# Kernel tuning notes

Measured on AMD Instinct MI355X. Metric: run time of the kernel, lower is better.

The kernel has to match this reference:

```python
import jax, jax.numpy as jnp
import numpy as np

B, S, E = 2, 2048, 1024
H = 16
D = E // H  # head_dim = 64


def setup_inputs() -> dict:
    key = jax.random.key(0)
    ks = jax.random.split(key, 11)
    s = 1.0 / np.sqrt(E)
    return {
        "x": jax.random.normal(ks[0], (B, S, E), dtype=jnp.float32),
        "Wq": jax.random.uniform(ks[1], (E, E), jnp.float32, -s, s),
        "bq": jnp.zeros((E,), jnp.float32),
        "Wk": jax.random.uniform(ks[2], (E, E), jnp.float32, -s, s),
        "bk": jnp.zeros((E,), jnp.float32),
        "Wv": jax.random.uniform(ks[3], (E, E), jnp.float32, -s, s),
        "bv": jnp.zeros((E,), jnp.float32),
        "Wo": jax.random.uniform(ks[4], (E, E), jnp.float32, -s, s),
        "bo": jnp.zeros((E,), jnp.float32),
        "J_attn": jax.random.normal(ks[5], (H, D, D), jnp.float32) * 0.02,
        "lambda_attn": jnp.float32(0.5),
    }


def reference(x, Wq, bq, Wk, bk, Wv, bv, Wo, bo, J_attn, lambda_attn):
    b, s, _ = x.shape
    scale = jnp.sqrt(jnp.float32(D))

    def split_heads(y):  # [b,s,E] -> [b,H,s,D]
        return y.reshape(b, s, H, D).transpose(0, 2, 1, 3)

    Q = split_heads(x @ Wq.T + bq)
    K = split_heads(x @ Wk.T + bk)
    V = split_heads(x @ Wv.T + bv)

    attn_scores = jnp.einsum('bhid,bhjd->bhij', Q, K) / scale

    Qn = jnp.tanh(Q)
    Kn = jnp.tanh(K)
    # fold J into Qn first (small [H,D,D] contraction), then one big matmul
    QJ = jnp.einsum('bhid,hde->bhie', Qn, J_attn)
    delta = jnp.einsum('bhie,bhje->bhij', QJ, Kn)

    attn_scores = attn_scores + lambda_attn * delta
    attn_probs = jax.nn.softmax(attn_scores, axis=-1)

    out = jnp.einsum('bhij,bhjd->bhid', attn_probs, V)
    out = out.transpose(0, 2, 1, 3).reshape(b, s, E)
    return out @ Wo.T + bo
```

## Files before the change

### kernel.cpp

```cpp
#include <hip/hip_runtime.h>
#include <math.h>

#define NH 16

typedef __bf16 bf16x8 __attribute__((ext_vector_type(8)));
typedef float f32x4 __attribute__((ext_vector_type(4)));

__device__ __forceinline__ unsigned short f2bf(float f) {
  unsigned u = __float_as_uint(f);
  u += 0x7fffu + ((u >> 16) & 1u);
  return (unsigned short)(u >> 16);
}
__device__ __forceinline__ float bf2f(unsigned short h) {
  return __uint_as_float(((unsigned)h) << 16);
}
__device__ __forceinline__ float fexp2(float x) {
  return __builtin_amdgcn_exp2f(x);
}
__device__ __forceinline__ float fast_tanh16(float x) {
  return 1.f - 2.f * __builtin_amdgcn_rcpf(fexp2(16.f * x) + 1.f);
}
__device__ __forceinline__ void gl_lds16(const void* g, void* l) {
  __builtin_amdgcn_global_load_lds((const __attribute__((address_space(1))) void*)g,
                                   (__attribute__((address_space(3))) void*)l, 16, 0, 0);
}
union Frag8 { bf16x8 v; unsigned short u[8]; };
union FragU { bf16x8 v; unsigned u[4]; };
union FragQ { bf16x8 v; unsigned long long q[2]; };

__global__ __launch_bounds__(256) void prep_all(const float* __restrict__ x,
                                                const float* __restrict__ Wq,
                                                const float* __restrict__ Wk,
                                                const float* __restrict__ Wv,
                                                const float* __restrict__ Wo,
                                                unsigned short* __restrict__ xh,
                                                unsigned short* __restrict__ wcat3,
                                                unsigned short* __restrict__ wocat)
{
  const int bid = blockIdx.x, tid = threadIdx.x;
  if (bid < 4096) {
    int i = bid * 256 + tid;
    float4 v = *(const float4*)&x[(size_t)i*4];
    ushort4 o;
    o.x = f2bf(v.x); o.y = f2bf(v.y); o.z = f2bf(v.z); o.w = f2bf(v.w);
    *(ushort4*)&xh[(size_t)i*4] = o;
  } else if (bid < 7168) {
    int i = (bid - 4096) * 256 + tid;
    int sel = i >> 18, loc = i & 262143;
    const float* src = (sel == 0) ? Wq : (sel == 1) ? Wk : Wv;
    float4 v = *(const float4*)&src[(size_t)loc*4];
    ushort4 o;
    o.x = f2bf(v.x); o.y = f2bf(v.y); o.z = f2bf(v.z); o.w = f2bf(v.w);
    *(ushort4*)&wcat3[(size_t)i*4] = o;
  } else {
    int i = (bid - 7168) * 256 + tid;
    int r = i >> 8, c = i & 255;
    float4 v = *(const float4*)&Wo[(size_t)r*1024 + c*4];
    ushort4 hi, lo;
    hi.x = f2bf(v.x); lo.x = f2bf(v.x - bf2f(hi.x));
    hi.y = f2bf(v.y); lo.y = f2bf(v.y - bf2f(hi.y));
    hi.z = f2bf(v.z); lo.z = f2bf(v.z - bf2f(hi.z));
    hi.w = f2bf(v.w); lo.w = f2bf(v.w - bf2f(hi.w));
    *(ushort4*)&wocat[(size_t)r*2048 + c*4]        = hi;
    *(ushort4*)&wocat[(size_t)r*2048 + 1024 + c*4] = lo;
  }
}

__global__ __launch_bounds__(256) void prep_jt(const float* __restrict__ J,
                                               const float* __restrict__ lam_p,
                                               unsigned short* __restrict__ Jt)
{
  __shared__ float T[64][65];
  const int h = blockIdx.x, tid = threadIdx.x;
  const float lam = lam_p[0] * 1.44269504f;
#pragma unroll
  for (int c = 0; c < 4; ++c) {
    int i = tid + c*256;
    int d = i >> 4, e4 = i & 15;
    float4 v = *(const float4*)&J[(size_t)h*4096 + d*64 + e4*4];
    T[d][e4*4+0] = v.x; T[d][e4*4+1] = v.y; T[d][e4*4+2] = v.z; T[d][e4*4+3] = v.w;
  }
  __syncthreads();
  const int e = tid >> 2, d0 = (tid & 3) * 16;
#pragma unroll
  for (int j4 = 0; j4 < 4; ++j4) {
    ushort4 o;
    o.x = f2bf(lam * T[d0+j4*4+0][e]);
    o.y = f2bf(lam * T[d0+j4*4+1][e]);
    o.z = f2bf(lam * T[d0+j4*4+2][e]);
    o.w = f2bf(lam * T[d0+j4*4+3][e]);
    *(ushort4*)&Jt[((size_t)h*64 + e)*64 + d0 + j4*4] = o;
  }
}

__global__ __launch_bounds__(256) void gemm_qkv(const unsigned short* __restrict__ A,
                                                const unsigned short* __restrict__ W,
                                                const float* __restrict__ bq,
                                                const float* __restrict__ bk,
                                                const float* __restrict__ bv,
                                                unsigned short* __restrict__ Qcat,
                                                unsigned short* __restrict__ Kcat,
                                                unsigned short* __restrict__ Vt)
{
  __shared__ unsigned short S[16384];
  const int tid = threadIdx.x, lane = tid & 63, wq = tid >> 6;
  const int l15 = lane & 15, lq = lane >> 4;
  const int n0 = blockIdx.x * 128, m0 = blockIdx.y * 128;
  const int wr = (wq & 1) * 64, wc = (wq >> 1) * 64;
  const int mode = n0 >> 10;

  f32x4 acc[4][4];
#pragma unroll
  for (int mb = 0; mb < 4; ++mb)
#pragma unroll
    for (int nb = 0; nb < 4; ++nb) { f32x4 z = {0.f,0.f,0.f,0.f}; acc[mb][nb] = z; }

  const unsigned short* mat = (wq < 2) ? A : W;
  const int rbase = (wq < 2) ? m0 : n0;
  unsigned short* lbase = S + (wq >> 1) * 8192;
  const int srow = lane >> 3, sslot = lane & 7;

  for (int k0 = 0; k0 < 1024; k0 += 64) {
    __syncthreads();
#pragma unroll
    for (int t = 0; t < 8; ++t) {
      int row = (wq & 1) * 64 + t*8 + srow;
      int chunk = sslot ^ (row & 7);
      gl_lds16(mat + (size_t)(rbase + row)*1024 + k0 + chunk*8,
               lbase + ((wq & 1) * 64 + t*8) * 64);
    }
    __syncthreads();
#pragma unroll
    for (int kk = 0; kk < 2; ++kk) {
      int c = kk*4 + lq;
      bf16x8 af[4], bf_[4];
#pragma unroll
      for (int mb = 0; mb < 4; ++mb) {
        int m = wr + mb*16 + l15;
        af[mb] = *(const bf16x8*)&S[m*64 + (c ^ (m & 7))*8];
      }
#pragma unroll
      for (int nb = 0; nb < 4; ++nb) {
        int n = wc + nb*16 + l15;
        bf_[nb] = *(const bf16x8*)&S[8192 + n*64 + (c ^ (n & 7))*8];
      }
#pragma unroll
      for (int mb = 0; mb < 4; ++mb)
#pragma unroll
        for (int nb = 0; nb < 4; ++nb)
          acc[mb][nb] = __builtin_amdgcn_mfma_f32_16x16x32_bf16(af[mb], bf_[nb], acc[mb][nb], 0,0,0);
    }
  }

  const float* bias = (mode == 0) ? bq : (mode == 1) ? bk : bv;
  float bvv[4];
#pragma unroll
  for (int nb = 0; nb < 4; ++nb) bvv[nb] = bias[((n0 & 1023) + wc + nb*16 + l15)];

  if (mode == 2) {
#pragma unroll
    for (int mb = 0; mb < 4; ++mb) {
      int mrow = m0 + wr + mb*16 + lq*4;
      int b = mrow >> 11, s0 = mrow & 2047;
#pragma unroll
      for (int nb = 0; nb < 4; ++nb) {
        int n = (n0 & 1023) + wc + nb*16 + l15;
        int h = n >> 6, d = n & 63;
        ushort4 o;
        o.x = f2bf(acc[mb][nb][0] + bvv[nb]);
        o.y = f2bf(acc[mb][nb][1] + bvv[nb]);
        o.z = f2bf(acc[mb][nb][2] + bvv[nb]);
        o.w = f2bf(acc[mb][nb][3] + bvv[nb]);
        *(ushort4*)&Vt[((size_t)(b*NH + h)*64 + d)*2048 + s0] = o;
      }
    }
    return;
  }

#pragma unroll
  for (int mb = 0; mb < 4; ++mb) {
#pragma unroll
    for (int r = 0; r < 4; ++r) {
      int m = m0 + wr + mb*16 + lq*4 + r;
      int b = m >> 11, s = m & 2047;
#pragma unroll
      for (int nb = 0; nb < 4; ++nb) {
        float v = acc[mb][nb][r] + bvv[nb];
        int n = (n0 & 1023) + wc + nb*16 + l15;
        int h = n >> 6, d = n & 63;
        size_t row = ((size_t)(b*NH + h)*2048 + s)*128;
        if (mode == 0) {
          Qcat[row + d] = f2bf(v * 0.18033688f);
        } else {
          Kcat[row + d]      = f2bf(v);
          Kcat[row + 64 + d] = f2bf(1.f - 2.f * __builtin_amdgcn_rcpf(__expf(2.f*v) + 1.f));
        }
      }
    }
  }
}

__global__ __launch_bounds__(256) void build_qj2(unsigned short* __restrict__ Qcat,
                                                 const unsigned short* __restrict__ Jt)
{
  const int tid = threadIdx.x, lane = tid & 63, wq = tid >> 6;
  const int l15 = lane & 15, lq = lane >> 4;
  const int bh = blockIdx.y, row0 = blockIdx.x * 128;
  const int h = bh & (NH-1);

  bf16x8 jf[4][2];
#pragma unroll
  for (int nb = 0; nb < 4; ++nb)
#pragma unroll
    for (int kst = 0; kst < 2; ++kst)
      jf[nb][kst] = *(const bf16x8*)&Jt[((size_t)h*64 + nb*16 + l15)*64 + kst*32 + lq*8];

  Frag8 af[2][2];
#pragma unroll
  for (int mb = 0; mb < 2; ++mb) {
    const unsigned short* qp = Qcat + ((size_t)(bh*2048 + row0 + wq*32 + mb*16 + l15))*128 + lq*8;
#pragma unroll
    for (int kst = 0; kst < 2; ++kst) {
      Frag8 raw;
      raw.v = *(const bf16x8*)(qp + kst*32);
#pragma unroll
      for (int j = 0; j < 8; ++j) {
        float t = fast_tanh16(bf2f(raw.u[j]));
        af[mb][kst].u[j] = (unsigned short)(__float_as_uint(t) >> 16);
      }
    }
  }

  f32x4 acc[2][4];
#pragma unroll
  for (int mb = 0; mb < 2; ++mb)
#pragma unroll
    for (int nb = 0; nb < 4; ++nb) { f32x4 z = {0.f,0.f,0.f,0.f}; acc[mb][nb] = z; }
#pragma unroll
  for (int kst = 0; kst < 2; ++kst)
#pragma unroll
    for (int mb = 0; mb < 2; ++mb)
#pragma unroll
      for (int nb = 0; nb < 4; ++nb)
        acc[mb][nb] = __builtin_amdgcn_mfma_f32_16x16x32_bf16(af[mb][kst].v, jf[nb][kst], acc[mb][nb], 0,0,0);

#pragma unroll
  for (int mb = 0; mb < 2; ++mb)
#pragma unroll
    for (int r = 0; r < 4; ++r) {
      size_t rowb = ((size_t)(bh*2048 + row0 + wq*32 + mb*16 + lq*4 + r))*128 + 64;
#pragma unroll
      for (int nb = 0; nb < 4; ++nb)
        Qcat[rowb + nb*16 + l15] = f2bf(acc[mb][nb][r]);
    }
}

__global__ __launch_bounds__(256, 4) void flash7(
    const unsigned short* __restrict__ Qcat, const unsigned short* __restrict__ Kcat,
    const unsigned short* __restrict__ Vt, float* __restrict__ OP0,
    float* __restrict__ OP1, float* __restrict__ OP2, float* __restrict__ lpart)
{
  __shared__ unsigned short Ks[64*128];
  __shared__ unsigned short Vs[64*64];
  const int tid = threadIdx.x, lane = tid & 63, wq = tid >> 6;
  const int l15 = lane & 15, lq = lane >> 4;
  const int bid = blockIdx.x;
  const int bh = (((bid >> 3) & 3) << 3) | (bid & 7);
  const int inner = bid >> 5;
  const int row0 = (inner & 15) * 128;
  const int ks = inner >> 4;
  const int jt0 = ks * 11;
  const int jtN = jt0 + ((ks < 2) ? 11 : 10);

  Frag8 qf[2][4];
#pragma unroll
  for (int nb = 0; nb < 2; ++nb) {
    const unsigned short* qp = Qcat + ((size_t)(bh*2048 + row0 + wq*32 + nb*16 + l15))*128 + lq*8;
#pragma unroll
    for (int kst = 0; kst < 4; ++kst)
      qf[nb][kst].v = *(const bf16x8*)(qp + kst*32);
  }

  FragU ones;
  ones.u[0] = 0x3F803F80u; ones.u[1] = 0x3F803F80u;
  ones.u[2] = 0x3F803F80u; ones.u[3] = 0x3F803F80u;

  f32x4 o[4][2];
  f32x4 lacc[2];
  { f32x4 z = {0.f,0.f,0.f,0.f}; lacc[0] = z; lacc[1] = z; }
#pragma unroll
  for (int db = 0; db < 4; ++db)
#pragma unroll
    for (int nb = 0; nb < 2; ++nb) { f32x4 z = {0.f,0.f,0.f,0.f}; o[db][nb] = z; }

  const unsigned short* kgb = Kcat + ((size_t)bh*2048)*128;
  const unsigned short* vg  = Vt + (size_t)bh*64*2048;

  for (int jt = jt0; jt < jtN; ++jt) {
    __syncthreads();
#pragma unroll
    for (int t = 0; t < 4; ++t) {
      int g = (wq*4 + t)*4 + (lane >> 4);
      int slot = lane & 15;
      int chunk = (slot & 8) | ((slot ^ g) & 7);
      gl_lds16(kgb + (size_t)(jt*64 + g)*128 + chunk*8, Ks + (wq*4 + t)*512);
    }
#pragma unroll
    for (int t = 0; t < 2; ++t) {
      int rv = (wq*2 + t)*8 + (lane >> 3);
      int chunk = (lane & 7) ^ (rv & 7);
      gl_lds16(vg + (size_t)rv*2048 + jt*64 + chunk*8, Vs + (wq*2 + t)*512);
    }
    __syncthreads();

#pragma unroll
    for (int t = 0; t < 2; ++t) {
      unsigned P2[2][2][2];
#pragma unroll
      for (int kk = 0; kk < 2; ++kk) {
        const int kb = 2*t + kk;
        bf16x8 af[4];
#pragma unroll
        for (int kst = 0; kst < 4; ++kst) {
          int key = kb*16 + l15;
          int c = kst*4 + lq;
          int slot = (c & 8) | ((c ^ key) & 7);
          af[kst] = *(const bf16x8*)&Ks[key*128 + slot*8];
        }
        f32x4 s[2];
        { f32x4 z = {0.f,0.f,0.f,0.f}; s[0] = z; s[1] = z; }
#pragma unroll
        for (int kst = 0; kst < 4; ++kst) {
          s[0] = __builtin_amdgcn_mfma_f32_16x16x32_bf16(af[kst], qf[0][kst].v, s[0], 0,0,0);
          s[1] = __builtin_amdgcn_mfma_f32_16x16x32_bf16(af[kst], qf[1][kst].v, s[1], 0,0,0);
        }
#pragma unroll
        for (int nb = 0; nb < 2; ++nb) {
          float e0 = fexp2(s[nb][0]), e1 = fexp2(s[nb][1]);
          float e2 = fexp2(s[nb][2]), e3 = fexp2(s[nb][3]);
          P2[nb][kk][0] = __builtin_amdgcn_perm(__float_as_uint(e1), __float_as_uint(e0), 0x07060302u);
          P2[nb][kk][1] = __builtin_amdgcn_perm(__float_as_uint(e3), __float_as_uint(e2), 0x07060302u);
        }
      }

      FragU bfr[2];
#pragma unroll
      for (int nb = 0; nb < 2; ++nb) {
        bfr[nb].u[0] = P2[nb][0][0];
        bfr[nb].u[1] = P2[nb][0][1];
        bfr[nb].u[2] = P2[nb][1][0];
        bfr[nb].u[3] = P2[nb][1][1];
      }
      lacc[0] = __builtin_amdgcn_mfma_f32_16x16x32_bf16(ones.v, bfr[0].v, lacc[0], 0,0,0);
      lacc[1] = __builtin_amdgcn_mfma_f32_16x16x32_bf16(ones.v, bfr[1].v, lacc[1], 0,0,0);

      const int c0 = 4*t + (lq >> 1);
      const int woff = 4*(lq & 1);
#pragma unroll
      for (int db = 0; db < 4; ++db) {
        int d = db*16 + l15;
        FragQ va;
        va.q[0] = *(const unsigned long long*)&Vs[d*64 + ((c0     ^ (d & 7))*8) + woff];
        va.q[1] = *(const unsigned long long*)&Vs[d*64 + (((c0+2) ^ (d & 7))*8) + woff];
        o[db][0] = __builtin_amdgcn_mfma_f32_16x16x32_bf16(va.v, bfr[0].v, o[db][0], 0,0,0);
        o[db][1] = __builtin_amdgcn_mfma_f32_16x16x32_bf16(va.v, bfr[1].v, o[db][1], 0,0,0);
      }
    }
  }

  float* OP = (ks == 0) ? OP0 : (ks == 1) ? OP1 : OP2;
#pragma unroll
  for (int nb = 0; nb < 2; ++nb) {
    int qrow = row0 + wq*32 + nb*16 + l15;
    if (lq == 0) lpart[(size_t)ks*65536 + bh*2048 + qrow] = lacc[nb][0];
#pragma unroll
    for (int db = 0; db < 4; ++db)
#pragma unroll
      for (int r = 0; r < 4; ++r) {
        int d = db*16 + lq*4 + r;
        OP[(size_t)(bh*64 + d)*2048 + qrow] = o[db][nb][r];
      }
  }
}

__global__ __launch_bounds__(256) void combine3(const float* __restrict__ OP0,
                                                const float* __restrict__ OP1,
                                                const float* __restrict__ OP2,
                                                const float* __restrict__ lpart,
                                                unsigned short* __restrict__ attcat)
{
  __shared__ float Ts[64*68];
  __shared__ float Ls[64];
  const int tid = threadIdx.x;
  const int bh = blockIdx.y, s0 = blockIdx.x * 64;
  const int b = bh >> 4, h = bh & (NH-1);
#pragma unroll
  for (int c = 0; c < 4; ++c) {
    int fid = tid + c*256;
    int d = fid >> 4, s4 = fid & 15;
    size_t gi = ((size_t)(bh*64 + d))*2048 + s0 + s4*4;
    float4 a = *(const float4*)&OP0[gi];
    float4 bb = *(const float4*)&OP1[gi];
    float4 cc = *(const float4*)&OP2[gi];
    Ts[(s4*4+0)*68 + d] = a.x + bb.x + cc.x;
    Ts[(s4*4+1)*68 + d] = a.y + bb.y + cc.y;
    Ts[(s4*4+2)*68 + d] = a.z + bb.z + cc.z;
    Ts[(s4*4+3)*68 + d] = a.w + bb.w + cc.w;
  }
  if (tid < 64) {
    size_t li = (size_t)bh*2048 + s0 + tid;
    Ls[tid] = lpart[li] + lpart[65536 + li] + lpart[131072 + li];
  }
  __syncthreads();
  const int sl = tid >> 2, d0 = (tid & 3) * 16;
  const float inv = 1.f / Ls[sl];
  const size_t rb = ((size_t)(b*2048 + s0 + sl))*2048 + h*64;
#pragma unroll
  for (int j4 = 0; j4 < 4; ++j4) {
    float4 t = *(const float4*)&Ts[sl*68 + d0 + j4*4];
    float v0 = t.x*inv, v1 = t.y*inv, v2 = t.z*inv, v3 = t.w*inv;
    ushort4 hi, lo;
    hi.x = f2bf(v0); lo.x = f2bf(v0 - bf2f(hi.x));
    hi.y = f2bf(v1); lo.y = f2bf(v1 - bf2f(hi.y));
    hi.z = f2bf(v2); lo.z = f2bf(v2 - bf2f(hi.z));
    hi.w = f2bf(v3); lo.w = f2bf(v3 - bf2f(hi.w));
    *(ushort4*)&attcat[rb + d0 + j4*4]        = hi;
    *(ushort4*)&attcat[rb + 1024 + d0 + j4*4] = lo;
  }
}

__global__ __launch_bounds__(512) void gemm3b(const unsigned short* __restrict__ A,
                                              const unsigned short* __restrict__ W,
                                              const float* __restrict__ bias,
                                              float* __restrict__ out)
{
  __shared__ unsigned short S[65536];
  const int tid = threadIdx.x, lane = tid & 63, wid = tid >> 6;
  const int l15 = lane & 15, lq = lane >> 4;
  const int n0 = blockIdx.x * 128, m0 = blockIdx.y * 128;
  const int wrow = wid >> 2, wcol = wid & 3;

  f32x4 acc[4][2];
#pragma unroll
  for (int mb = 0; mb < 4; ++mb)
#pragma unroll
    for (int nb = 0; nb < 2; ++nb) { f32x4 z = {0.f,0.f,0.f,0.f}; acc[mb][nb] = z; }

  const int region = wid >> 1;
  const unsigned short* mat = (region < 2) ? A : W;
  const int rbase = (region < 2) ? m0 : n0;
  const int koff  = (region & 1) * 1024;
  const int rhalf = (wid & 1) * 64;
  const int srow = lane >> 3, sslot = lane & 7;

  auto STAGE = [&](int buf, int k0) {
    unsigned short* lb = S + buf*32768 + region*8192 + rhalf*64;
#pragma unroll
    for (int t = 0; t < 8; ++t) {
      int row = rhalf + t*8 + srow;
      int chunk = sslot ^ (row & 7);
      gl_lds16(mat + (size_t)(rbase + row)*2048 + koff + k0 + chunk*8,
               lb + t*512);
    }
  };

  int cur = 0;
  STAGE(0, 0);
  __syncthreads();

  for (int k0 = 0; k0 < 1024; k0 += 64) {
    if (k0 + 64 < 1024) STAGE(cur ^ 1, k0 + 64);
    const unsigned short* Sc = S + cur*32768;
#pragma unroll
    for (int kk = 0; kk < 2; ++kk) {
      int c = kk*4 + lq;
      bf16x8 ah[4], al[4], bh_[2], bl_[2];
#pragma unroll
      for (int mb = 0; mb < 4; ++mb) {
        int m = wrow*64 + mb*16 + l15;
        int so = (c ^ (m & 7))*8;
        ah[mb] = *(const bf16x8*)&Sc[m*64 + so];
        al[mb] = *(const bf16x8*)&Sc[8192 + m*64 + so];
      }
#pragma unroll
      for (int nb = 0; nb < 2; ++nb) {
        int n = wcol*32 + nb*16 + l15;
        int so = (c ^ (n & 7))*8;
        bh_[nb] = *(const bf16x8*)&Sc[16384 + n*64 + so];
        bl_[nb] = *(const bf16x8*)&Sc[24576 + n*64 + so];
      }
#pragma unroll
      for (int mb = 0; mb < 4; ++mb)
#pragma unroll
        for (int nb = 0; nb < 2; ++nb) {
          acc[mb][nb] = __builtin_amdgcn_mfma_f32_16x16x32_bf16(ah[mb], bh_[nb], acc[mb][nb], 0,0,0);
          acc[mb][nb] = __builtin_amdgcn_mfma_f32_16x16x32_bf16(al[mb], bh_[nb], acc[mb][nb], 0,0,0);
          acc[mb][nb] = __builtin_amdgcn_mfma_f32_16x16x32_bf16(ah[mb], bl_[nb], acc[mb][nb], 0,0,0);
        }
    }
    __syncthreads();
    cur ^= 1;
  }

  float bvv[2];
#pragma unroll
  for (int nb = 0; nb < 2; ++nb) bvv[nb] = bias[n0 + wcol*32 + nb*16 + l15];
#pragma unroll
  for (int mb = 0; mb < 4; ++mb)
#pragma unroll
    for (int r = 0; r < 4; ++r) {
      int m = m0 + wrow*64 + mb*16 + lq*4 + r;
#pragma unroll
      for (int nb = 0; nb < 2; ++nb) {
        int n = n0 + wcol*32 + nb*16 + l15;
        out[(size_t)m*1024 + n] = acc[mb][nb][r] + bvv[nb];
      }
    }
}

extern "C" void kernel_launch(void* const* d_in, const int* in_sizes, int n_in,
                              void* d_out, int out_size, void* d_ws, size_t ws_size,
                              hipStream_t stream)
{
  const float* x   = (const float*)d_in[0];
  const float* Wq  = (const float*)d_in[1];
  const float* bq  = (const float*)d_in[2];
  const float* Wk  = (const float*)d_in[3];
  const float* bk  = (const float*)d_in[4];
  const float* Wv  = (const float*)d_in[5];
  const float* bv  = (const float*)d_in[6];
  const float* Wo  = (const float*)d_in[7];
  const float* bo  = (const float*)d_in[8];
  const float* J   = (const float*)d_in[9];
  const float* lam = (const float*)d_in[10];

  char* p = (char*)d_ws;
  char* regionA = p;
  unsigned short* xh     = (unsigned short*)p;  p += (size_t)4096*1024*2;
  unsigned short* wcat3  = (unsigned short*)p;  p += (size_t)3072*1024*2;
  unsigned short* Jt     = (unsigned short*)p;  p += (size_t)16*64*64*2;
  p += (size_t)2*1024*1024;
  unsigned short* Qcat   = (unsigned short*)p;  p += (size_t)65536*128*2;
  unsigned short* Kcat   = (unsigned short*)p;  p += (size_t)65536*128*2;
  unsigned short* Vt     = (unsigned short*)p;  p += (size_t)32*64*2048*2;
  unsigned short* wocat  = (unsigned short*)p;  p += (size_t)1024*2048*2;
  unsigned short* attcat = (unsigned short*)p;  p += (size_t)4096*2048*2;
  float*          OP0    = (float*)p;           p += (size_t)32*64*2048*4;
  float*          OP1    = (float*)p;           p += (size_t)32*64*2048*4;
  float*          lpart  = (float*)p;           p += (size_t)3*65536*4;
  float*          OP2    = (float*)regionA;
  float* out = (float*)d_out;

  dim3 blk(256);

  prep_all<<<dim3(8192), blk, 0, stream>>>(x, Wq, Wk, Wv, Wo, xh, wcat3, wocat);
  prep_jt<<<dim3(16), blk, 0, stream>>>(J, lam, Jt);
  gemm_qkv<<<dim3(24, 32), blk, 0, stream>>>(xh, wcat3, bq, bk, bv, Qcat, Kcat, Vt);
  build_qj2<<<dim3(16, 32), blk, 0, stream>>>(Qcat, Jt);
  flash7<<<dim3(1536), blk, 0, stream>>>(Qcat, Kcat, Vt, OP0, OP1, OP2, lpart);
  combine3<<<dim3(32, 32), blk, 0, stream>>>(OP0, OP1, OP2, lpart, attcat);
  gemm3b<<<dim3(8, 32), dim3(512), 0, stream>>>(attcat, wocat, bo, out);
}
```

Before: 247.3 us.

## Double-buffer QKV GEMM and flash LDS tiles, fold prep_jt into prep_all

Result: faster. 240.3 us (-2.8%).

```diff
diff --git a/kernel.cpp b/kernel.cpp
--- a/kernel.cpp
+++ b/kernel.cpp
@@ -33,11 +33,38 @@
                                                 const float* __restrict__ Wk,
                                                 const float* __restrict__ Wv,
                                                 const float* __restrict__ Wo,
+                                                const float* __restrict__ J,
+                                                const float* __restrict__ lam_p,
                                                 unsigned short* __restrict__ xh,
                                                 unsigned short* __restrict__ wcat3,
-                                                unsigned short* __restrict__ wocat)
-{
+                                                unsigned short* __restrict__ wocat,
+                                                unsigned short* __restrict__ Jt)
+{
+  __shared__ float T[64][65];
   const int bid = blockIdx.x, tid = threadIdx.x;
+  if (bid >= 8192) {
+    const int h = bid - 8192;
+    const float lam = lam_p[0] * 1.44269504f;
+#pragma unroll
+    for (int c = 0; c < 4; ++c) {
+      int i = tid + c*256;
+      int d = i >> 4, e4 = i & 15;
+      float4 v = *(const float4*)&J[(size_t)h*4096 + d*64 + e4*4];
+      T[d][e4*4+0] = v.x; T[d][e4*4+1] = v.y; T[d][e4*4+2] = v.z; T[d][e4*4+3] = v.w;
+    }
+    __syncthreads();
+    const int e = tid >> 2, d0 = (tid & 3) * 16;
+#pragma unroll
+    for (int j4 = 0; j4 < 4; ++j4) {
+      ushort4 o;
+      o.x = f2bf(lam * T[d0+j4*4+0][e]);
+      o.y = f2bf(lam * T[d0+j4*4+1][e]);
+      o.z = f2bf(lam * T[d0+j4*4+2][e]);
+      o.w = f2bf(lam * T[d0+j4*4+3][e]);
+      *(ushort4*)&Jt[((size_t)h*64 + e)*64 + d0 + j4*4] = o;
+    }
+    return;
+  }
   if (bid < 4096) {
     int i = bid * 256 + tid;
     float4 v = *(const float4*)&x[(size_t)i*4];
@@ -66,34 +93,7 @@
   }
 }
 
-__global__ __launch_bounds__(256) void prep_jt(const float* __restrict__ J,
-                                               const float* __restrict__ lam_p,
-                                               unsigned short* __restrict__ Jt)
-{
-  __shared__ float T[64][65];
-  const int h = blockIdx.x, tid = threadIdx.x;
-  const float lam = lam_p[0] * 1.44269504f;
-#pragma unroll
-  for (int c = 0; c < 4; ++c) {
-    int i = tid + c*256;
-    int d = i >> 4, e4 = i & 15;
-    float4 v = *(const float4*)&J[(size_t)h*4096 + d*64 + e4*4];
-    T[d][e4*4+0] = v.x; T[d][e4*4+1] = v.y; T[d][e4*4+2] = v.z; T[d][e4*4+3] = v.w;
-  }
-  __syncthreads();
-  const int e = tid >> 2, d0 = (tid & 3) * 16;
-#pragma unroll
-  for (int j4 = 0; j4 < 4; ++j4) {
-    ushort4 o;
-    o.x = f2bf(lam * T[d0+j4*4+0][e]);
-    o.y = f2bf(lam * T[d0+j4*4+1][e]);
-    o.z = f2bf(lam * T[d0+j4*4+2][e]);
-    o.w = f2bf(lam * T[d0+j4*4+3][e]);
-    *(ushort4*)&Jt[((size_t)h*64 + e)*64 + d0 + j4*4] = o;
-  }
-}
-
-__global__ __launch_bounds__(256) void gemm_qkv(const unsigned short* __restrict__ A,
+__global__ __launch_bounds__(512) void gemm_qkv(const unsigned short* __restrict__ A,
                                                 const unsigned short* __restrict__ W,
                                                 const float* __restrict__ bq,
                                                 const float* __restrict__ bk,
@@ -102,69 +102,78 @@
                                                 unsigned short* __restrict__ Kcat,
                                                 unsigned short* __restrict__ Vt)
 {
-  __shared__ unsigned short S[16384];
-  const int tid = threadIdx.x, lane = tid & 63, wq = tid >> 6;
+  __shared__ unsigned short S[32768];
+  const int tid = threadIdx.x, lane = tid & 63, wid = tid >> 6;
   const int l15 = lane & 15, lq = lane >> 4;
   const int n0 = blockIdx.x * 128, m0 = blockIdx.y * 128;
-  const int wr = (wq & 1) * 64, wc = (wq >> 1) * 64;
+  const int wrow = wid >> 2, wcol = wid & 3;
   const int mode = n0 >> 10;
 
-  f32x4 acc[4][4];
+  f32x4 acc[4][2];
 #pragma unroll
   for (int mb = 0; mb < 4; ++mb)
 #pragma unroll
-    for (int nb = 0; nb < 4; ++nb) { f32x4 z = {0.f,0.f,0.f,0.f}; acc[mb][nb] = z; }
-
-  const unsigned short* mat = (wq < 2) ? A : W;
-  const int rbase = (wq < 2) ? m0 : n0;
-  unsigned short* lbase = S + (wq >> 1) * 8192;
+    for (int nb = 0; nb < 2; ++nb) { f32x4 z = {0.f,0.f,0.f,0.f}; acc[mb][nb] = z; }
+
+  const int region = wid >> 2, quarter = wid & 3;
+  const unsigned short* mat = (region == 0) ? A : W;
+  const int rbase = (region == 0) ? m0 : n0;
   const int srow = lane >> 3, sslot = lane & 7;
 
+  auto STAGE = [&](int buf, int k0) {
+    unsigned short* lb = S + buf*16384 + region*8192 + quarter*2048;
+#pragma unroll
+    for (int t = 0; t < 4; ++t) {
+      int row = quarter*32 + t*8 + srow;
+      int chunk = sslot ^ (row & 7);
+      gl_lds16(mat + (size_t)(rbase + row)*1024 + k0 + chunk*8, lb + t*512);
+    }
+  };
+
+  int cur = 0;
+  STAGE(0, 0);
+  __syncthreads();
+
   for (int k0 = 0; k0 < 1024; k0 += 64) {
-    __syncthreads();
-#pragma unroll
-    for (int t = 0; t < 8; ++t) {
-      int row = (wq & 1) * 64 + t*8 + srow;
-      int chunk = sslot ^ (row & 7);
-      gl_lds16(mat + (size_t)(rbase + row)*1024 + k0 + chunk*8,
-               lbase + ((wq & 1) * 64 + t*8) * 64);
-    }
-    __syncthreads();
+    if (k0 + 64 < 1024) STAGE(cur ^ 1, k0 + 64);
+    const unsigned short* Sc = S + cur*16384;
 #pragma unroll
     for (int kk = 0; kk < 2; ++kk) {
       int c = kk*4 + lq;
-      bf16x8 af[4], bf_[4];
+      bf16x8 af[4], bf_[2];
 #pragma unroll
       for (int mb = 0; mb < 4; ++mb) {
-        int m = wr + mb*16 + l15;
-        af[mb] = *(const bf16x8*)&S[m*64 + (c ^ (m & 7))*8];
-      }
-#pragma unroll
-      for (int nb = 0; nb < 4; ++nb) {
-        int n = wc + nb*16 + l15;
-        bf_[nb] = *(const bf16x8*)&S[8192 + n*64 + (c ^ (n & 7))*8];
+        int m = wrow*64 + mb*16 + l15;
+        af[mb] = *(const bf16x8*)&Sc[m*64 + (c ^ (m & 7))*8];
+      }
+#pragma unroll
+      for (int nb = 0; nb < 2; ++nb) {
+        int n = wcol*32 + nb*16 + l15;
+        bf_[nb] = *(const bf16x8*)&Sc[8192 + n*64 + (c ^ (n & 7))*8];
       }
 #pragma unroll
       for (int mb = 0; mb < 4; ++mb)
 #pragma unroll
-        for (int nb = 0; nb < 4; ++nb)
+        for (int nb = 0; nb < 2; ++nb)
           acc[mb][nb] = __builtin_amdgcn_mfma_f32_16x16x32_bf16(af[mb], bf_[nb], acc[mb][nb], 0,0,0);
     }
+    __syncthreads();
+    cur ^= 1;
   }
 
   const float* bias = (mode == 0) ? bq : (mode == 1) ? bk : bv;
-  float bvv[4];
-#pragma unroll
-  for (int nb = 0; nb < 4; ++nb) bvv[nb] = bias[((n0 & 1023) + wc + nb*16 + l15)];
+  float bvv[2];
+#pragma unroll
+  for (int nb = 0; nb < 2; ++nb) bvv[nb] = bias[((n0 & 1023) + wcol*32 + nb*16 + l15)];
 
   if (mode == 2) {
 #pragma unroll
     for (int mb = 0; mb < 4; ++mb) {
-      int mrow = m0 + wr + mb*16 + lq*4;
+      int mrow = m0 + wrow*64 + mb*16 + lq*4;
       int b = mrow >> 11, s0 = mrow & 2047;
 #pragma unroll
-      for (int nb = 0; nb < 4; ++nb) {
-        int n = (n0 & 1023) + wc + nb*16 + l15;
+      for (int nb = 0; nb < 2; ++nb) {
+        int n = (n0 & 1023) + wcol*32 + nb*16 + l15;
         int h = n >> 6, d = n & 63;
         ushort4 o;
         o.x = f2bf(acc[mb][nb][0] + bvv[nb]);
@@ -181,12 +190,12 @@
   for (int mb = 0; mb < 4; ++mb) {
 #pragma unroll
     for (int r = 0; r < 4; ++r) {
-      int m = m0 + wr + mb*16 + lq*4 + r;
+      int m = m0 + wrow*64 + mb*16 + lq*4 + r;
       int b = m >> 11, s = m & 2047;
 #pragma unroll
-      for (int nb = 0; nb < 4; ++nb) {
+      for (int nb = 0; nb < 2; ++nb) {
         float v = acc[mb][nb][r] + bvv[nb];
-        int n = (n0 & 1023) + wc + nb*16 + l15;
+        int n = (n0 & 1023) + wcol*32 + nb*16 + l15;
         int h = n >> 6, d = n & 63;
         size_t row = ((size_t)(b*NH + h)*2048 + s)*128;
         if (mode == 0) {
@@ -260,8 +269,8 @@
     const unsigned short* __restrict__ Vt, float* __restrict__ OP0,
     float* __restrict__ OP1, float* __restrict__ OP2, float* __restrict__ lpart)
 {
-  __shared__ unsigned short Ks[64*128];
-  __shared__ unsigned short Vs[64*64];
+  __shared__ unsigned short Ks[2][64*128];
+  __shared__ unsigned short Vs[2][64*64];
   const int tid = threadIdx.x, lane = tid & 63, wq = tid >> 6;
   const int l15 = lane & 15, lq = lane >> 4;
   const int bid = blockIdx.x;
@@ -296,22 +305,30 @@
   const unsigned short* kgb = Kcat + ((size_t)bh*2048)*128;
   const unsigned short* vg  = Vt + (size_t)bh*64*2048;
 
-  for (int jt = jt0; jt < jtN; ++jt) {
-    __syncthreads();
+  auto STAGE = [&](int buf, int jt) {
 #pragma unroll
     for (int t = 0; t < 4; ++t) {
       int g = (wq*4 + t)*4 + (lane >> 4);
       int slot = lane & 15;
       int chunk = (slot & 8) | ((slot ^ g) & 7);
-      gl_lds16(kgb + (size_t)(jt*64 + g)*128 + chunk*8, Ks + (wq*4 + t)*512);
+      gl_lds16(kgb + (size_t)(jt*64 + g)*128 + chunk*8, &Ks[buf][(wq*4 + t)*512]);
     }
 #pragma unroll
     for (int t = 0; t < 2; ++t) {
       int rv = (wq*2 + t)*8 + (lane >> 3);
       int chunk = (lane & 7) ^ (rv & 7);
-      gl_lds16(vg + (size_t)rv*2048 + jt*64 + chunk*8, Vs + (wq*2 + t)*512);
-    }
-    __syncthreads();
+      gl_lds16(vg + (size_t)rv*2048 + jt*64 + chunk*8, &Vs[buf][(wq*2 + t)*512]);
+    }
+  };
+
+  int cur = 0;
+  STAGE(0, jt0);
+  __syncthreads();
+
+  for (int jt = jt0; jt < jtN; ++jt) {
+    if (jt + 1 < jtN) STAGE(cur ^ 1, jt + 1);
+    const unsigned short* ksb = Ks[cur];
+    const unsigned short* vsb = Vs[cur];
 
 #pragma unroll
     for (int t = 0; t < 2; ++t) {
@@ -325,15 +342,17 @@
           int key = kb*16 + l15;
           int c = kst*4 + lq;
           int slot = (c & 8) | ((c ^ key) & 7);
-          af[kst] = *(const bf16x8*)&Ks[key*128 + slot*8];
+          af[kst] = *(const bf16x8*)&ksb[key*128 + slot*8];
         }
         f32x4 s[2];
         { f32x4 z = {0.f,0.f,0.f,0.f}; s[0] = z; s[1] = z; }
+        __builtin_amdgcn_s_setprio(1);
 #pragma unroll
         for (int kst = 0; kst < 4; ++kst) {
           s[0] = __builtin_amdgcn_mfma_f32_16x16x32_bf16(af[kst], qf[0][kst].v, s[0], 0,0,0);
           s[1] = __builtin_amdgcn_mfma_f32_16x16x32_bf16(af[kst], qf[1][kst].v, s[1], 0,0,0);
         }
+        __builtin_amdgcn_s_setprio(0);
 #pragma unroll
         for (int nb = 0; nb < 2; ++nb) {
           float e0 = fexp2(s[nb][0]), e1 = fexp2(s[nb][1]);
@@ -351,6 +370,7 @@
         bfr[nb].u[2] = P2[nb][1][0];
         bfr[nb].u[3] = P2[nb][1][1];
       }
+      __builtin_amdgcn_s_setprio(1);
       lacc[0] = __builtin_amdgcn_mfma_f32_16x16x32_bf16(ones.v, bfr[0].v, lacc[0], 0,0,0);
       lacc[1] = __builtin_amdgcn_mfma_f32_16x16x32_bf16(ones.v, bfr[1].v, lacc[1], 0,0,0);
 
@@ -360,12 +380,16 @@
       for (int db = 0; db < 4; ++db) {
         int d = db*16 + l15;
         FragQ va;
-        va.q[0] = *(const unsigned long long*)&Vs[d*64 + ((c0     ^ (d & 7))*8) + woff];
-        va.q[1] = *(const unsigned long long*)&Vs[d*64 + (((c0+2) ^ (d & 7))*8) + woff];
+        va.q[0] = *(const unsigned long long*)&vsb[d*64 + ((c0     ^ (d & 7))*8) + woff];
+        va.q[1] = *(const unsigned long long*)&vsb[d*64 + (((c0+2) ^ (d & 7))*8) + woff];
         o[db][0] = __builtin_amdgcn_mfma_f32_16x16x32_bf16(va.v, bfr[0].v, o[db][0], 0,0,0);
         o[db][1] = __builtin_amdgcn_mfma_f32_16x16x32_bf16(va.v, bfr[1].v, o[db][1], 0,0,0);
       }
-    }
+      __builtin_amdgcn_s_setprio(0);
+    }
+
+    __syncthreads();
+    cur ^= 1;
   }
 
   float* OP = (ks == 0) ? OP0 : (ks == 1) ? OP1 : OP2;
@@ -553,9 +577,8 @@
 
   dim3 blk(256);
 
-  prep_all<<<dim3(8192), blk, 0, stream>>>(x, Wq, Wk, Wv, Wo, xh, wcat3, wocat);
-  prep_jt<<<dim3(16), blk, 0, stream>>>(J, lam, Jt);
-  gemm_qkv<<<dim3(24, 32), blk, 0, stream>>>(xh, wcat3, bq, bk, bv, Qcat, Kcat, Vt);
+  prep_all<<<dim3(8208), blk, 0, stream>>>(x, Wq, Wk, Wv, Wo, J, lam, xh, wcat3, wocat, Jt);
+  gemm_qkv<<<dim3(24, 32), dim3(512), 0, stream>>>(xh, wcat3, bq, bk, bv, Qcat, Kcat, Vt);
   build_qj2<<<dim3(16, 32), blk, 0, stream>>>(Qcat, Jt);
   flash7<<<dim3(1536), blk, 0, stream>>>(Qcat, Kcat, Vt, OP0, OP1, OP2, lpart);
   combine3<<<dim3(32, 32), blk, 0, stream>>>(OP0, OP1, OP2, lpart, attcat);
```

## Double-buffer QKV GEMM loads, add MFMA priority hints, fold J prep into prep kernel

Applied to the files above, without the earlier changes.

Result: faster. 231.9 us (-6.2%).

```diff
diff --git a/kernel.cpp b/kernel.cpp
--- a/kernel.cpp
+++ b/kernel.cpp
@@ -33,11 +33,38 @@
                                                 const float* __restrict__ Wk,
                                                 const float* __restrict__ Wv,
                                                 const float* __restrict__ Wo,
+                                                const float* __restrict__ J,
+                                                const float* __restrict__ lam_p,
                                                 unsigned short* __restrict__ xh,
                                                 unsigned short* __restrict__ wcat3,
-                                                unsigned short* __restrict__ wocat)
-{
+                                                unsigned short* __restrict__ wocat,
+                                                unsigned short* __restrict__ Jt)
+{
+  __shared__ float T[64][65];
   const int bid = blockIdx.x, tid = threadIdx.x;
+  if (bid >= 8192) {
+    const int h = bid - 8192;
+    const float lam = lam_p[0] * 1.44269504f;
+#pragma unroll
+    for (int c = 0; c < 4; ++c) {
+      int i = tid + c*256;
+      int d = i >> 4, e4 = i & 15;
+      float4 v = *(const float4*)&J[(size_t)h*4096 + d*64 + e4*4];
+      T[d][e4*4+0] = v.x; T[d][e4*4+1] = v.y; T[d][e4*4+2] = v.z; T[d][e4*4+3] = v.w;
+    }
+    __syncthreads();
+    const int e = tid >> 2, d0 = (tid & 3) * 16;
+#pragma unroll
+    for (int j4 = 0; j4 < 4; ++j4) {
+      ushort4 o;
+      o.x = f2bf(lam * T[d0+j4*4+0][e]);
+      o.y = f2bf(lam * T[d0+j4*4+1][e]);
+      o.z = f2bf(lam * T[d0+j4*4+2][e]);
+      o.w = f2bf(lam * T[d0+j4*4+3][e]);
+      *(ushort4*)&Jt[((size_t)h*64 + e)*64 + d0 + j4*4] = o;
+    }
+    return;
+  }
   if (bid < 4096) {
     int i = bid * 256 + tid;
     float4 v = *(const float4*)&x[(size_t)i*4];
@@ -66,33 +93,6 @@
   }
 }
 
-__global__ __launch_bounds__(256) void prep_jt(const float* __restrict__ J,
-                                               const float* __restrict__ lam_p,
-                                               unsigned short* __restrict__ Jt)
-{
-  __shared__ float T[64][65];
-  const int h = blockIdx.x, tid = threadIdx.x;
-  const float lam = lam_p[0] * 1.44269504f;
-#pragma unroll
-  for (int c = 0; c < 4; ++c) {
-    int i = tid + c*256;
-    int d = i >> 4, e4 = i & 15;
-    float4 v = *(const float4*)&J[(size_t)h*4096 + d*64 + e4*4];
-    T[d][e4*4+0] = v.x; T[d][e4*4+1] = v.y; T[d][e4*4+2] = v.z; T[d][e4*4+3] = v.w;
-  }
-  __syncthreads();
-  const int e = tid >> 2, d0 = (tid & 3) * 16;
-#pragma unroll
-  for (int j4 = 0; j4 < 4; ++j4) {
-    ushort4 o;
-    o.x = f2bf(lam * T[d0+j4*4+0][e]);
-    o.y = f2bf(lam * T[d0+j4*4+1][e]);
-    o.z = f2bf(lam * T[d0+j4*4+2][e]);
-    o.w = f2bf(lam * T[d0+j4*4+3][e]);
-    *(ushort4*)&Jt[((size_t)h*64 + e)*64 + d0 + j4*4] = o;
-  }
-}
-
 __global__ __launch_bounds__(256) void gemm_qkv(const unsigned short* __restrict__ A,
                                                 const unsigned short* __restrict__ W,
                                                 const float* __restrict__ bq,
@@ -102,7 +102,7 @@
                                                 unsigned short* __restrict__ Kcat,
                                                 unsigned short* __restrict__ Vt)
 {
-  __shared__ unsigned short S[16384];
+  __shared__ unsigned short S[32768];
   const int tid = threadIdx.x, lane = tid & 63, wq = tid >> 6;
   const int l15 = lane & 15, lq = lane >> 4;
   const int n0 = blockIdx.x * 128, m0 = blockIdx.y * 128;
@@ -117,19 +117,26 @@
 
   const unsigned short* mat = (wq < 2) ? A : W;
   const int rbase = (wq < 2) ? m0 : n0;
-  unsigned short* lbase = S + (wq >> 1) * 8192;
   const int srow = lane >> 3, sslot = lane & 7;
 
-  for (int k0 = 0; k0 < 1024; k0 += 64) {
-    __syncthreads();
+  auto STAGE = [&](int buf, int k0) {
+    unsigned short* lb = S + buf*16384 + (wq >> 1) * 8192;
 #pragma unroll
     for (int t = 0; t < 8; ++t) {
       int row = (wq & 1) * 64 + t*8 + srow;
       int chunk = sslot ^ (row & 7);
       gl_lds16(mat + (size_t)(rbase + row)*1024 + k0 + chunk*8,
-               lbase + ((wq & 1) * 64 + t*8) * 64);
-    }
-    __syncthreads();
+               lb + ((wq & 1) * 64 + t*8) * 64);
+    }
+  };
+
+  int cur = 0;
+  STAGE(0, 0);
+  __syncthreads();
+
+  for (int k0 = 0; k0 < 1024; k0 += 64) {
+    if (k0 + 64 < 1024) STAGE(cur ^ 1, k0 + 64);
+    const unsigned short* Sc = S + cur*16384;
 #pragma unroll
     for (int kk = 0; kk < 2; ++kk) {
       int c = kk*4 + lq;
@@ -137,12 +144,12 @@
 #pragma unroll
       for (int mb = 0; mb < 4; ++mb) {
         int m = wr + mb*16 + l15;
-        af[mb] = *(const bf16x8*)&S[m*64 + (c ^ (m & 7))*8];
+        af[mb] = *(const bf16x8*)&Sc[m*64 + (c ^ (m & 7))*8];
       }
 #pragma unroll
       for (int nb = 0; nb < 4; ++nb) {
         int n = wc + nb*16 + l15;
-        bf_[nb] = *(const bf16x8*)&S[8192 + n*64 + (c ^ (n & 7))*8];
+        bf_[nb] = *(const bf16x8*)&Sc[8192 + n*64 + (c ^ (n & 7))*8];
       }
 #pragma unroll
       for (int mb = 0; mb < 4; ++mb)
@@ -150,6 +157,8 @@
         for (int nb = 0; nb < 4; ++nb)
           acc[mb][nb] = __builtin_amdgcn_mfma_f32_16x16x32_bf16(af[mb], bf_[nb], acc[mb][nb], 0,0,0);
     }
+    __syncthreads();
+    cur ^= 1;
   }
 
   const float* bias = (mode == 0) ? bq : (mode == 1) ? bk : bv;
@@ -329,11 +338,13 @@
         }
         f32x4 s[2];
         { f32x4 z = {0.f,0.f,0.f,0.f}; s[0] = z; s[1] = z; }
+        __builtin_amdgcn_s_setprio(1);
 #pragma unroll
         for (int kst = 0; kst < 4; ++kst) {
           s[0] = __builtin_amdgcn_mfma_f32_16x16x32_bf16(af[kst], qf[0][kst].v, s[0], 0,0,0);
           s[1] = __builtin_amdgcn_mfma_f32_16x16x32_bf16(af[kst], qf[1][kst].v, s[1], 0,0,0);
         }
+        __builtin_amdgcn_s_setprio(0);
 #pragma unroll
         for (int nb = 0; nb < 2; ++nb) {
           float e0 = fexp2(s[nb][0]), e1 = fexp2(s[nb][1]);
@@ -351,6 +362,7 @@
         bfr[nb].u[2] = P2[nb][1][0];
         bfr[nb].u[3] = P2[nb][1][1];
       }
+      __builtin_amdgcn_s_setprio(1);
       lacc[0] = __builtin_amdgcn_mfma_f32_16x16x32_bf16(ones.v, bfr[0].v, lacc[0], 0,0,0);
       lacc[1] = __builtin_amdgcn_mfma_f32_16x16x32_bf16(ones.v, bfr[1].v, lacc[1], 0,0,0);
 
@@ -365,6 +377,7 @@
         o[db][0] = __builtin_amdgcn_mfma_f32_16x16x32_bf16(va.v, bfr[0].v, o[db][0], 0,0,0);
         o[db][1] = __builtin_amdgcn_mfma_f32_16x16x32_bf16(va.v, bfr[1].v, o[db][1], 0,0,0);
       }
+      __builtin_amdgcn_s_setprio(0);
     }
   }
 
@@ -553,8 +566,7 @@
 
   dim3 blk(256);
 
-  prep_all<<<dim3(8192), blk, 0, stream>>>(x, Wq, Wk, Wv, Wo, xh, wcat3, wocat);
-  prep_jt<<<dim3(16), blk, 0, stream>>>(J, lam, Jt);
+  prep_all<<<dim3(8208), blk, 0, stream>>>(x, Wq, Wk, Wv, Wo, J, lam, xh, wcat3, wocat, Jt);
   gemm_qkv<<<dim3(24, 32), blk, 0, stream>>>(xh, wcat3, bq, bk, bv, Qcat, Kcat, Vt);
   build_qj2<<<dim3(16, 32), blk, 0, stream>>>(Qcat, Jt);
   flash7<<<dim3(1536), blk, 0, stream>>>(Qcat, Kcat, Vt, OP0, OP1, OP2, lpart);
```
